# Optimization experiments

Hardware: AMD Instinct MI355X
Metric: run time of the kernel (lower is better)

The kernel has to match this reference:

```python
import math
import jax, jax.numpy as jnp
import numpy as np

B, S, D, H, DH, R, V = 8, 1024, 1024, 8, 512, 36, 32002  # DH = d_model//2, HD = h*DH = 4096
HD = H * DH
LN_EPS = 1e-5


def setup_inputs() -> dict:
    key = jax.random.key(0)
    ks = jax.random.split(key, 16)

    def n(k, shp, std=0.02):
        return jax.random.normal(k, shp, jnp.float32) * std

    pre_words = jax.random.randint(ks[0], (B, S), 0, V)
    img_features = jax.random.normal(ks[1], (B, R, D), jnp.float32)
    exp_embed = n(ks[2], (V, D)).at[0].set(0.0)  # padding_idx=0
    # id2visual table: sparse nonneg rows over 36 regions; zero rows -> textual tokens
    id2vis = (jax.random.uniform(ks[3], (V, R)) < 0.05).astype(jnp.float32)
    # stacked params for 2 transformer layers; weights stored (in, out) so y = x @ W + b
    wq = n(ks[4], (2, D, HD)); bq = jnp.zeros((2, HD), jnp.float32)
    wk = n(ks[5], (2, D, HD)); bk = jnp.zeros((2, HD), jnp.float32)
    wv = n(ks[6], (2, D, HD)); bv = jnp.zeros((2, HD), jnp.float32)
    wo = n(ks[7], (2, HD, D)); bo = jnp.zeros((2, D), jnp.float32)
    w1 = n(ks[8], (2, D, D)); b1 = jnp.zeros((2, D), jnp.float32)
    w2 = n(ks[9], (2, D, D)); b2 = jnp.zeros((2, D), jnp.float32)
    ln1_g = jnp.ones((2, D), jnp.float32); ln1_b = jnp.zeros((2, D), jnp.float32)
    ln2_g = jnp.ones((2, D), jnp.float32); ln2_b = jnp.zeros((2, D), jnp.float32)
    return dict(pre_words=pre_words, img_features=img_features, exp_embed=exp_embed,
                id2vis=id2vis, wq=wq, bq=bq, wk=wk, bk=bk, wv=wv, bv=bv, wo=wo, bo=bo,
                w1=w1, b1=b1, w2=w2, b2=b2, ln1_g=ln1_g, ln1_b=ln1_b, ln2_g=ln2_g, ln2_b=ln2_b)


def _layer_norm(x, g, b):
    m = x.mean(-1, keepdims=True)
    v = ((x - m) ** 2).mean(-1, keepdims=True)
    return (x - m) / jnp.sqrt(v + LN_EPS) * g + b


def _softmax_one(x):
    # shifted-denominator softmax: exp(x - max) / (1 + sum exp(x - max))
    x = x - x.max(-1, keepdims=True)
    e = jnp.exp(x)
    return e / (1.0 + e.sum(-1, keepdims=True))


def reference(pre_words, img_features, exp_embed, id2vis, wq, bq, wk, bk, wv, bv,
              wo, bo, w1, b1, w2, b2, ln1_g, ln1_b, ln2_g, ln2_b):
    # token embedding: textual (masked to 0 where a visual row exists) + visual bmm
    te = exp_embed[pre_words]                       # (B,S,D)
    vids = id2vis[pre_words]                        # (B,S,R)
    word_mask = vids.sum(-1, keepdims=True) != 0    # (B,S,1)
    ve = jnp.einsum('bsr,brd->bsd', vids, img_features)
    x = jnp.where(word_mask, 0.0, te) + ve          # (B,S,D)

    scale = 1.0 / math.sqrt(DH)
    for i in range(2):  # two structurally identical transformer layers
        h = _layer_norm(x, ln1_g[i], ln1_b[i])
        q = (h @ wq[i] + bq[i]).reshape(B, S, H, DH).transpose(0, 2, 1, 3)
        k = (h @ wk[i] + bk[i]).reshape(B, S, H, DH).transpose(0, 2, 1, 3)
        v = (h @ wv[i] + bv[i]).reshape(B, S, H, DH).transpose(0, 2, 1, 3)
        attn = _softmax_one(jnp.einsum('bhqd,bhkd->bhqk', q, k) * scale)  # (B,H,S,S)
        o = jnp.einsum('bhqk,bhkd->bhqd', attn, v)
        o = o.transpose(0, 2, 1, 3).reshape(B, S, HD)
        x = x + (o @ wo[i] + bo[i])
        f = _layer_norm(x, ln2_g[i], ln2_b[i])
        f = jax.nn.gelu(f @ w1[i] + b1[i], approximate=False) @ w2[i] + b2[i]
        x = x + f
    return x
```

## Files before the change

kernel.cpp:

```cpp
#include <hip/hip_runtime.h>


using u16 = unsigned short;
typedef __attribute__((ext_vector_type(8))) short bf16x8;
typedef __attribute__((ext_vector_type(4))) float f32x4;

__device__ __forceinline__ float b2f(u16 u) {
  union { unsigned int i; float f; } v; v.i = ((unsigned int)u) << 16; return v.f;
}
__device__ __forceinline__ u16 f2b(float f) {
  union { float f; unsigned int i; } v; v.f = f;
  unsigned int i = v.i;
  return (u16)((i + 0x7FFFu + ((i >> 16) & 1u)) >> 16);
}
__device__ __forceinline__ float gelu_f(float x) {
  return 0.5f * x * (1.f + erff(x * 0.70710678118654752f));
}
__device__ __forceinline__ void async16(void* lds, const void* g) {
  __builtin_amdgcn_global_load_lds((const __attribute__((address_space(1))) void*)g,
                                   (__attribute__((address_space(3))) void*)lds, 16, 0, 0);
}
__device__ __forceinline__ void storeC(float* p, float v) { *p = v; }
__device__ __forceinline__ void storeC(u16* p, float v) { *p = f2b(v); }

__global__ __launch_bounds__(256) void embed_k(
    const int* __restrict__ words, const float* __restrict__ img,
    const float* __restrict__ emb, const float* __restrict__ id2v,
    float* __restrict__ x)
{
  __shared__ float vs[36];
  int tok = blockIdx.x, b = tok >> 10, t = threadIdx.x;
  int wd = words[tok];
  if (t < 36) vs[t] = id2v[(size_t)wd * 36 + t];
  __syncthreads();
  bool any = false;
#pragma unroll
  for (int r = 0; r < 36; ++r) any = any || (vs[r] != 0.f);
#pragma unroll
  for (int i = 0; i < 4; ++i) {
    int d = t + (i << 8);
    float acc = 0.f;
    for (int r = 0; r < 36; ++r) {
      float vv = vs[r];
      if (vv != 0.f) acc += vv * img[((size_t)(b * 36 + r) << 10) + d];
    }
    float te = any ? 0.f : emb[((size_t)wd << 10) + d];
    x[((size_t)tok << 10) + d] = te + acc;
  }
}

__global__ __launch_bounds__(256) void ln_k(
    const float* __restrict__ x, u16* __restrict__ out,
    const float* __restrict__ g, const float* __restrict__ bb)
{
  __shared__ float red[4];
  int row = blockIdx.x, t = threadIdx.x;
  const float* xr = x + ((size_t)row << 10);
  float v[4], s = 0.f;
#pragma unroll
  for (int i = 0; i < 4; ++i) { v[i] = xr[t + (i << 8)]; s += v[i]; }
#pragma unroll
  for (int o = 32; o; o >>= 1) s += __shfl_xor(s, o, 64);
  if ((t & 63) == 0) red[t >> 6] = s;
  __syncthreads();
  s = red[0] + red[1] + red[2] + red[3];
  float mean = s * 0.0009765625f;
  float q = 0.f;
#pragma unroll
  for (int i = 0; i < 4; ++i) { float d = v[i] - mean; q += d * d; }
  __syncthreads();
#pragma unroll
  for (int o = 32; o; o >>= 1) q += __shfl_xor(q, o, 64);
  if ((t & 63) == 0) red[t >> 6] = q;
  __syncthreads();
  q = red[0] + red[1] + red[2] + red[3];
  float rstd = rsqrtf(q * 0.0009765625f + 1e-5f);
  u16* orow = out + ((size_t)row << 10);
#pragma unroll
  for (int i = 0; i < 4; ++i) {
    int d = t + (i << 8);
    orow[d] = f2b((v[i] - mean) * rstd * g[d] + bb[d]);
  }
}

__global__ __launch_bounds__(256) void sm_k(const float* __restrict__ S, u16* __restrict__ P)
{
  __shared__ float red[4];
  size_t row = blockIdx.x;
  int t = threadIdx.x;
  const float* sr = S + (row << 10);
  float v[4], m = -3.0e38f;
#pragma unroll
  for (int i = 0; i < 4; ++i) { v[i] = sr[t + (i << 8)]; m = fmaxf(m, v[i]); }
#pragma unroll
  for (int o = 32; o; o >>= 1) m = fmaxf(m, __shfl_xor(m, o, 64));
  if ((t & 63) == 0) red[t >> 6] = m;
  __syncthreads();
  m = fmaxf(fmaxf(red[0], red[1]), fmaxf(red[2], red[3]));
  float e[4], s = 0.f;
#pragma unroll
  for (int i = 0; i < 4; ++i) { e[i] = __expf(v[i] - m); s += e[i]; }
  __syncthreads();
#pragma unroll
  for (int o = 32; o; o >>= 1) s += __shfl_xor(s, o, 64);
  if ((t & 63) == 0) red[t >> 6] = s;
  __syncthreads();
  s = red[0] + red[1] + red[2] + red[3];
  float inv = 1.f / (1.f + s);
  u16* pr = P + (row << 10);
#pragma unroll
  for (int i = 0; i < 4; ++i) pr[t + (i << 8)] = f2b(e[i] * inv);
}

__global__ __launch_bounds__(256) void tr_k(
    const float* __restrict__ src, u16* __restrict__ dst, int ls, int ld)
{
  __shared__ u16 tile[64][65];
  int c0 = blockIdx.x << 6, r0 = blockIdx.y << 6;
  int tx = threadIdx.x & 63, ty0 = threadIdx.x >> 6;
#pragma unroll
  for (int i = 0; i < 16; ++i) {
    int ty = (ty0 << 4) + i;
    tile[ty][tx] = f2b(src[(size_t)(r0 + ty) * ls + (c0 + tx)]);
  }
  __syncthreads();
#pragma unroll
  for (int i = 0; i < 16; ++i) {
    int ty = (ty0 << 4) + i;
    dst[(size_t)(c0 + ty) * ld + (r0 + tx)] = tile[tx][ty];
  }
}

template <typename CT, int ACT, int BIAS, int RESID>
__global__ __launch_bounds__(256, 4) void gemm128(
    const u16* __restrict__ A, const u16* __restrict__ Bt,
    CT* __restrict__ C, const float* __restrict__ bias,
    const float* __restrict__ resid,
    int M, int N, int K, int lda, int ldb, int ldc, float scale,
    int zbase, int zdiv, int ga, int gb, int gc,
    long long aS1, long long aS2, long long bS1, long long bS2,
    long long cS1, long long cS2)
{
  __shared__ u16 lA[128 * 64];
  __shared__ u16 lB[128 * 64];
  const int nwg = gridDim.x * gridDim.y;
  const int id = blockIdx.y * gridDim.x + blockIdx.x;
  const int qq = nwg >> 3, rr8 = nwg & 7;
  const int xcd = id & 7, off = id >> 3;
  const int swz = (xcd < rr8 ? xcd * (qq + 1) : rr8 * (qq + 1) + (xcd - rr8) * qq) + off;
  const int bx = swz % gridDim.x, by = swz / gridDim.x;

  long long lz = blockIdx.z;
  long long gz = zbase + lz;
  long long zA = ga ? gz : lz, zB = gb ? gz : lz, zC = gc ? gz : lz;
  size_t aOff = (size_t)((zA / zdiv) * aS1 + (zA % zdiv) * aS2);
  size_t bOff = (size_t)((zB / zdiv) * bS1 + (zB % zdiv) * bS2);
  size_t cOff = (size_t)((zC / zdiv) * cS1 + (zC % zdiv) * cS2);
  const int m0 = by << 7, n0 = bx << 7;
  const int tid = threadIdx.x, lane = tid & 63, w = tid >> 6;
  const int wm = w >> 1, wn = w & 1;
  const int srow8 = lane >> 3;
  const int schunk = (lane & 7) ^ srow8;
  const int fr = lane & 15, hi = lane >> 4;

  f32x4 acc[4][4];
#pragma unroll
  for (int mi = 0; mi < 4; ++mi)
#pragma unroll
    for (int ni = 0; ni < 4; ++ni) acc[mi][ni] = 0.f;

  const u16* Ab = A + aOff;
  const u16* Bb = Bt + bOff;

  for (int k0 = 0; k0 < K; k0 += 64) {
#pragma unroll
    for (int s = 0; s < 4; ++s) {
      const int rb = (s << 5) + (w << 3);
      async16(&lA[rb << 6], Ab + (size_t)(m0 + rb + srow8) * lda + (k0 + (schunk << 3)));
      async16(&lB[rb << 6], Bb + (size_t)(n0 + rb + srow8) * ldb + (k0 + (schunk << 3)));
    }
    __syncthreads();
#pragma unroll
    for (int ks = 0; ks < 2; ++ks) {
      const int q = (ks << 2) + hi;
      bf16x8 a8[4], b8[4];
#pragma unroll
      for (int mi = 0; mi < 4; ++mi) {
        const int R = (wm << 6) + (mi << 4) + fr;
        a8[mi] = *(const bf16x8*)&lA[(R << 6) + ((q ^ (R & 7)) << 3)];
      }
#pragma unroll
      for (int ni = 0; ni < 4; ++ni) {
        const int R = (wn << 6) + (ni << 4) + fr;
        b8[ni] = *(const bf16x8*)&lB[(R << 6) + ((q ^ (R & 7)) << 3)];
      }
#pragma unroll
      for (int mi = 0; mi < 4; ++mi)
#pragma unroll
        for (int ni = 0; ni < 4; ++ni)
          acc[mi][ni] = __builtin_amdgcn_mfma_f32_16x16x32_bf16(a8[mi], b8[ni], acc[mi][ni], 0, 0, 0);
    }
    __syncthreads();
  }

  const int r4 = hi << 2, cc = fr;
#pragma unroll
  for (int mi = 0; mi < 4; ++mi) {
#pragma unroll
    for (int ni = 0; ni < 4; ++ni) {
      const int col = n0 + (wn << 6) + (ni << 4) + cc;
      float bcol = 0.f;
      if (BIAS == 1) bcol = bias[col];
#pragma unroll
      for (int j = 0; j < 4; ++j) {
        const int row = m0 + (wm << 6) + (mi << 4) + r4 + j;
        float v = acc[mi][ni][j] * scale + bcol;
        if (BIAS == 2) v += bias[row];
        if (ACT == 1) v = gelu_f(v);
        const size_t idx = cOff + (size_t)row * ldc + col;
        if (RESID) v += resid[idx];
        storeC(&C[idx], v);
      }
    }
  }
}

extern "C" void kernel_launch(void* const* d_in, const int* in_sizes, int n_in,
                              void* d_out, int out_size, void* d_ws, size_t ws_size,
                              hipStream_t stream)
{
  (void)in_sizes; (void)n_in; (void)out_size;
  const int*   pre_words = (const int*)d_in[0];
  const float* img  = (const float*)d_in[1];
  const float* emb  = (const float*)d_in[2];
  const float* id2v = (const float*)d_in[3];
  const float* wq = (const float*)d_in[4];  const float* bq = (const float*)d_in[5];
  const float* wk = (const float*)d_in[6];  const float* bk = (const float*)d_in[7];
  const float* wv = (const float*)d_in[8];  const float* bv = (const float*)d_in[9];
  const float* wo = (const float*)d_in[10]; const float* bo = (const float*)d_in[11];
  const float* w1 = (const float*)d_in[12]; const float* b1 = (const float*)d_in[13];
  const float* w2 = (const float*)d_in[14]; const float* b2 = (const float*)d_in[15];
  const float* ln1g = (const float*)d_in[16]; const float* ln1b = (const float*)d_in[17];
  const float* ln2g = (const float*)d_in[18]; const float* ln2b = (const float*)d_in[19];

  const size_t FIXED = 88080384 + (size_t)(1 << 16);
  int g = 1;
  for (int c = 8; c >= 1; c >>= 1)
    if (FIXED + (size_t)c * 33554432 + 6291456 <= ws_size) { g = c; break; }
  int nc = 1;
  int ncmax = 8 * g > 32 ? 32 : 8 * g;
  for (int c = ncmax; c >= 1; c >>= 1)
    if (FIXED + (size_t)g * 33554432 + (size_t)c * 6291456 <= ws_size) { nc = c; break; }

  char* p = (char*)d_ws;
  auto alloc = [&](size_t bytes) -> void* {
    void* r = (void*)p; p += (bytes + 255) & ~(size_t)255; return r;
  };
  float* x  = (float*)alloc((size_t)8192 * 1024 * 4);
  u16* h    = (u16*)alloc((size_t)8192 * 1024 * 2);
  u16* Qg   = (u16*)alloc((size_t)g * 1024 * 4096 * 2);
  u16* Og   = (u16*)alloc((size_t)g * 1024 * 4096 * 2);
  u16* ff   = Qg;
  u16* Kg   = (u16*)alloc((size_t)g * 1024 * 4096 * 2);
  u16* Vtg  = (u16*)alloc((size_t)g * 4096 * 1024 * 2);
  u16* wqt  = (u16*)alloc((size_t)4096 * 1024 * 2);
  u16* wkt  = (u16*)alloc((size_t)4096 * 1024 * 2);
  u16* wvt  = (u16*)alloc((size_t)4096 * 1024 * 2);
  u16* wot  = (u16*)alloc((size_t)1024 * 4096 * 2);
  u16* w1t  = (u16*)alloc((size_t)1024 * 1024 * 2);
  u16* w2t  = (u16*)alloc((size_t)1024 * 1024 * 2);
  float* Sc = (float*)alloc((size_t)nc << 22);
  u16*  Pp  = (u16*)alloc((size_t)nc << 21);

  embed_k<<<8192, 256, 0, stream>>>(pre_words, img, emb, id2v, x);

  const float qk_scale = 0.044194173824159216f;
  for (int L = 0; L < 2; ++L) {
    const float* WQ = wq + (size_t)L * 1024 * 4096;
    const float* WK = wk + (size_t)L * 1024 * 4096;
    const float* WV = wv + (size_t)L * 1024 * 4096;
    const float* WO = wo + (size_t)L * 4096 * 1024;
    const float* W1 = w1 + (size_t)L * 1024 * 1024;
    const float* W2 = w2 + (size_t)L * 1024 * 1024;

    tr_k<<<dim3(64, 16), 256, 0, stream>>>(WQ, wqt, 4096, 1024);
    tr_k<<<dim3(64, 16), 256, 0, stream>>>(WK, wkt, 4096, 1024);
    tr_k<<<dim3(64, 16), 256, 0, stream>>>(WV, wvt, 4096, 1024);
    tr_k<<<dim3(16, 64), 256, 0, stream>>>(WO, wot, 1024, 4096);
    tr_k<<<dim3(16, 16), 256, 0, stream>>>(W1, w1t, 1024, 1024);
    tr_k<<<dim3(16, 16), 256, 0, stream>>>(W2, w2t, 1024, 1024);

    ln_k<<<8192, 256, 0, stream>>>(x, h, ln1g + L * 1024, ln1b + L * 1024);

    for (int g0 = 0; g0 < 8; g0 += g) {
      const u16* hg = h + (size_t)g0 * 1048576;
      const int Mg = 1024 * g;
      gemm128<u16, 0, 1, 0><<<dim3(32, Mg >> 7), 256, 0, stream>>>(
          hg, wqt, Qg, bq + (size_t)L * 4096, nullptr,
          Mg, 4096, 1024, 1024, 1024, 4096, 1.f,
          0, 1, 0, 0, 0, 0, 0, 0, 0, 0, 0);
      gemm128<u16, 0, 1, 0><<<dim3(32, Mg >> 7), 256, 0, stream>>>(
          hg, wkt, Kg, bk + (size_t)L * 4096, nullptr,
          Mg, 4096, 1024, 1024, 1024, 4096, 1.f,
          0, 1, 0, 0, 0, 0, 0, 0, 0, 0, 0);
      gemm128<u16, 0, 2, 0><<<dim3(8, 32, g), 256, 0, stream>>>(
          wvt, h, Vtg, bv + (size_t)L * 4096, nullptr,
          4096, 1024, 1024, 1024, 1024, 1024, 1.f,
          g0, 1, 0, 1, 0, 0, 0, 1048576LL, 0, 4194304LL, 0);
      for (int c0 = 0; c0 < 8 * g; c0 += nc) {
        gemm128<float, 0, 0, 0><<<dim3(8, 8, nc), 256, 0, stream>>>(
            Qg, Kg, Sc, nullptr, nullptr,
            1024, 1024, 512, 4096, 4096, 1024, qk_scale,
            c0, 8, 1, 1, 0,
            4194304LL, 512LL, 4194304LL, 512LL, 8388608LL, 1048576LL);
        sm_k<<<nc << 10, 256, 0, stream>>>(Sc, Pp);
        gemm128<u16, 0, 0, 0><<<dim3(4, 8, nc), 256, 0, stream>>>(
            Pp, Vtg, Og, nullptr, nullptr,
            1024, 512, 1024, 1024, 1024, 4096, 1.f,
            c0, 8, 0, 1, 1,
            8388608LL, 1048576LL, 4194304LL, 524288LL, 4194304LL, 512LL);
      }
      gemm128<float, 0, 1, 1><<<dim3(8, Mg >> 7), 256, 0, stream>>>(
          Og, wot, x + (size_t)g0 * 1048576, bo + (size_t)L * 1024,
          x + (size_t)g0 * 1048576,
          Mg, 1024, 4096, 4096, 4096, 1024, 1.f,
          0, 1, 0, 0, 0, 0, 0, 0, 0, 0, 0);
    }

    ln_k<<<8192, 256, 0, stream>>>(x, h, ln2g + L * 1024, ln2b + L * 1024);

    gemm128<u16, 1, 1, 0><<<dim3(8, 64), 256, 0, stream>>>(
        h, w1t, ff, b1 + (size_t)L * 1024, nullptr,
        8192, 1024, 1024, 1024, 1024, 1024, 1.f,
        0, 1, 0, 0, 0, 0, 0, 0, 0, 0, 0);
    float* cdst = (L == 1) ? (float*)d_out : x;
    gemm128<float, 0, 1, 1><<<dim3(8, 64), 256, 0, stream>>>(
        ff, w2t, cdst, b2 + (size_t)L * 1024, x,
        8192, 1024, 1024, 1024, 1024, 1024, 1.f,
        0, 1, 0, 0, 0, 0, 0, 0, 0, 0, 0);
  }
}
```

Before: 1.655 ms.

## Store attention scores in bf16, vectorize softmax, add 128x64 GEMM tiles

The QK^T score buffer is now written as bf16 instead of fp32, which halves score write and softmax read traffic and frees workspace for larger chunk counts. The softmax kernel now loads and stores four contiguous elements per thread with ushort4. The GEMM is templated on N-tile width: N=1024 projections (Wo, FFN) use 128x64 tiles for more workgroups, and launch-bound occupancy hints are raised. Rounding scores to bf16 before softmax adds some precision loss.

```diff
diff --git a/kernel.cpp b/kernel.cpp
--- a/kernel.cpp
+++ b/kernel.cpp
@@ -83,15 +83,15 @@
   }
 }
 
-__global__ __launch_bounds__(256) void sm_k(const float* __restrict__ S, u16* __restrict__ P)
+__global__ __launch_bounds__(256) void sm_k(const u16* __restrict__ S, u16* __restrict__ P)
 {
   __shared__ float red[4];
   size_t row = blockIdx.x;
   int t = threadIdx.x;
-  const float* sr = S + (row << 10);
-  float v[4], m = -3.0e38f;
-#pragma unroll
-  for (int i = 0; i < 4; ++i) { v[i] = sr[t + (i << 8)]; m = fmaxf(m, v[i]); }
+  const u16* sr = S + (row << 10);
+  ushort4 sv = *(const ushort4*)(sr + (t << 2));
+  float v[4] = { b2f(sv.x), b2f(sv.y), b2f(sv.z), b2f(sv.w) };
+  float m = fmaxf(fmaxf(v[0], v[1]), fmaxf(v[2], v[3]));
 #pragma unroll
   for (int o = 32; o; o >>= 1) m = fmaxf(m, __shfl_xor(m, o, 64));
   if ((t & 63) == 0) red[t >> 6] = m;
@@ -107,9 +107,10 @@
   __syncthreads();
   s = red[0] + red[1] + red[2] + red[3];
   float inv = 1.f / (1.f + s);
-  u16* pr = P + (row << 10);
-#pragma unroll
-  for (int i = 0; i < 4; ++i) pr[t + (i << 8)] = f2b(e[i] * inv);
+  ushort4 pv;
+  pv.x = f2b(e[0] * inv); pv.y = f2b(e[1] * inv);
+  pv.z = f2b(e[2] * inv); pv.w = f2b(e[3] * inv);
+  *(ushort4*)(P + (row << 10) + (t << 2)) = pv;
 }
 
 __global__ __launch_bounds__(256) void tr_k(
@@ -131,8 +132,8 @@
   }
 }
 
-template <typename CT, int ACT, int BIAS, int RESID>
-__global__ __launch_bounds__(256, 4) void gemm128(
+template <typename CT, int ACT, int BIAS, int RESID, int BN>
+__global__ __launch_bounds__(256, (BN == 128) ? 5 : 6) void gemm_t(
     const u16* __restrict__ A, const u16* __restrict__ Bt,
     CT* __restrict__ C, const float* __restrict__ bias,
     const float* __restrict__ resid,
@@ -141,8 +142,9 @@
     long long aS1, long long aS2, long long bS1, long long bS2,
     long long cS1, long long cS2)
 {
+  constexpr int NACC = BN / 32;
   __shared__ u16 lA[128 * 64];
-  __shared__ u16 lB[128 * 64];
+  __shared__ u16 lB[BN * 64];
   const int nwg = gridDim.x * gridDim.y;
   const int id = blockIdx.y * gridDim.x + blockIdx.x;
   const int qq = nwg >> 3, rr8 = nwg & 7;
@@ -156,18 +158,18 @@
   size_t aOff = (size_t)((zA / zdiv) * aS1 + (zA % zdiv) * aS2);
   size_t bOff = (size_t)((zB / zdiv) * bS1 + (zB % zdiv) * bS2);
   size_t cOff = (size_t)((zC / zdiv) * cS1 + (zC % zdiv) * cS2);
-  const int m0 = by << 7, n0 = bx << 7;
+  const int m0 = by << 7, n0 = bx * BN;
   const int tid = threadIdx.x, lane = tid & 63, w = tid >> 6;
   const int wm = w >> 1, wn = w & 1;
   const int srow8 = lane >> 3;
   const int schunk = (lane & 7) ^ srow8;
   const int fr = lane & 15, hi = lane >> 4;
 
-  f32x4 acc[4][4];
+  f32x4 acc[4][NACC];
 #pragma unroll
   for (int mi = 0; mi < 4; ++mi)
 #pragma unroll
-    for (int ni = 0; ni < 4; ++ni) acc[mi][ni] = 0.f;
+    for (int ni = 0; ni < NACC; ++ni) acc[mi][ni] = 0.f;
 
   const u16* Ab = A + aOff;
   const u16* Bb = Bt + bOff;
@@ -177,27 +179,31 @@
     for (int s = 0; s < 4; ++s) {
       const int rb = (s << 5) + (w << 3);
       async16(&lA[rb << 6], Ab + (size_t)(m0 + rb + srow8) * lda + (k0 + (schunk << 3)));
+    }
+#pragma unroll
+    for (int s = 0; s < BN / 32; ++s) {
+      const int rb = (s << 5) + (w << 3);
       async16(&lB[rb << 6], Bb + (size_t)(n0 + rb + srow8) * ldb + (k0 + (schunk << 3)));
     }
     __syncthreads();
 #pragma unroll
     for (int ks = 0; ks < 2; ++ks) {
       const int q = (ks << 2) + hi;
-      bf16x8 a8[4], b8[4];
+      bf16x8 a8[4], b8[NACC];
 #pragma unroll
       for (int mi = 0; mi < 4; ++mi) {
         const int R = (wm << 6) + (mi << 4) + fr;
         a8[mi] = *(const bf16x8*)&lA[(R << 6) + ((q ^ (R & 7)) << 3)];
       }
 #pragma unroll
-      for (int ni = 0; ni < 4; ++ni) {
-        const int R = (wn << 6) + (ni << 4) + fr;
+      for (int ni = 0; ni < NACC; ++ni) {
+        const int R = wn * (BN / 2) + (ni << 4) + fr;
         b8[ni] = *(const bf16x8*)&lB[(R << 6) + ((q ^ (R & 7)) << 3)];
       }
 #pragma unroll
       for (int mi = 0; mi < 4; ++mi)
 #pragma unroll
-        for (int ni = 0; ni < 4; ++ni)
+        for (int ni = 0; ni < NACC; ++ni)
           acc[mi][ni] = __builtin_amdgcn_mfma_f32_16x16x32_bf16(a8[mi], b8[ni], acc[mi][ni], 0, 0, 0);
     }
     __syncthreads();
@@ -207,8 +213,8 @@
 #pragma unroll
   for (int mi = 0; mi < 4; ++mi) {
 #pragma unroll
-    for (int ni = 0; ni < 4; ++ni) {
-      const int col = n0 + (wn << 6) + (ni << 4) + cc;
+    for (int ni = 0; ni < NACC; ++ni) {
+      const int col = n0 + wn * (BN / 2) + (ni << 4) + cc;
       float bcol = 0.f;
       if (BIAS == 1) bcol = bias[col];
 #pragma unroll
@@ -246,11 +252,11 @@
   const size_t FIXED = 88080384 + (size_t)(1 << 16);
   int g = 1;
   for (int c = 8; c >= 1; c >>= 1)
-    if (FIXED + (size_t)c * 33554432 + 6291456 <= ws_size) { g = c; break; }
+    if (FIXED + (size_t)c * 33554432 + 4194304 <= ws_size) { g = c; break; }
   int nc = 1;
   int ncmax = 8 * g > 32 ? 32 : 8 * g;
   for (int c = ncmax; c >= 1; c >>= 1)
-    if (FIXED + (size_t)g * 33554432 + (size_t)c * 6291456 <= ws_size) { nc = c; break; }
+    if (FIXED + (size_t)g * 33554432 + (size_t)c * 4194304 <= ws_size) { nc = c; break; }
 
   char* p = (char*)d_ws;
   auto alloc = [&](size_t bytes) -> void* {
@@ -269,8 +275,8 @@
   u16* wot  = (u16*)alloc((size_t)1024 * 4096 * 2);
   u16* w1t  = (u16*)alloc((size_t)1024 * 1024 * 2);
   u16* w2t  = (u16*)alloc((size_t)1024 * 1024 * 2);
-  float* Sc = (float*)alloc((size_t)nc << 22);
-  u16*  Pp  = (u16*)alloc((size_t)nc << 21);
+  u16* Sc   = (u16*)alloc((size_t)nc << 21);
+  u16* Pp   = (u16*)alloc((size_t)nc << 21);
 
   embed_k<<<8192, 256, 0, stream>>>(pre_words, img, emb, id2v, x);
 
@@ -295,32 +301,32 @@
     for (int g0 = 0; g0 < 8; g0 += g) {
       const u16* hg = h + (size_t)g0 * 1048576;
       const int Mg = 1024 * g;
-      gemm128<u16, 0, 1, 0><<<dim3(32, Mg >> 7), 256, 0, stream>>>(
+      gemm_t<u16, 0, 1, 0, 128><<<dim3(32, Mg >> 7), 256, 0, stream>>>(
           hg, wqt, Qg, bq + (size_t)L * 4096, nullptr,
           Mg, 4096, 1024, 1024, 1024, 4096, 1.f,
           0, 1, 0, 0, 0, 0, 0, 0, 0, 0, 0);
-      gemm128<u16, 0, 1, 0><<<dim3(32, Mg >> 7), 256, 0, stream>>>(
+      gemm_t<u16, 0, 1, 0, 128><<<dim3(32, Mg >> 7), 256, 0, stream>>>(
           hg, wkt, Kg, bk + (size_t)L * 4096, nullptr,
           Mg, 4096, 1024, 1024, 1024, 4096, 1.f,
           0, 1, 0, 0, 0, 0, 0, 0, 0, 0, 0);
-      gemm128<u16, 0, 2, 0><<<dim3(8, 32, g), 256, 0, stream>>>(
+      gemm_t<u16, 0, 2, 0, 128><<<dim3(8, 32, g), 256, 0, stream>>>(
           wvt, h, Vtg, bv + (size_t)L * 4096, nullptr,
           4096, 1024, 1024, 1024, 1024, 1024, 1.f,
           g0, 1, 0, 1, 0, 0, 0, 1048576LL, 0, 4194304LL, 0);
       for (int c0 = 0; c0 < 8 * g; c0 += nc) {
-        gemm128<float, 0, 0, 0><<<dim3(8, 8, nc), 256, 0, stream>>>(
+        gemm_t<u16, 0, 0, 0, 128><<<dim3(8, 8, nc), 256, 0, stream>>>(
             Qg, Kg, Sc, nullptr, nullptr,
             1024, 1024, 512, 4096, 4096, 1024, qk_scale,
             c0, 8, 1, 1, 0,
             4194304LL, 512LL, 4194304LL, 512LL, 8388608LL, 1048576LL);
         sm_k<<<nc << 10, 256, 0, stream>>>(Sc, Pp);
-        gemm128<u16, 0, 0, 0><<<dim3(4, 8, nc), 256, 0, stream>>>(
+        gemm_t<u16, 0, 0, 0, 128><<<dim3(4, 8, nc), 256, 0, stream>>>(
             Pp, Vtg, Og, nullptr, nullptr,
             1024, 512, 1024, 1024, 1024, 4096, 1.f,
             c0, 8, 0, 1, 1,
             8388608LL, 1048576LL, 4194304LL, 524288LL, 4194304LL, 512LL);
       }
-      gemm128<float, 0, 1, 1><<<dim3(8, Mg >> 7), 256, 0, stream>>>(
+      gemm_t<float, 0, 1, 1, 64><<<dim3(16, Mg >> 7), 256, 0, stream>>>(
           Og, wot, x + (size_t)g0 * 1048576, bo + (size_t)L * 1024,
           x + (size_t)g0 * 1048576,
           Mg, 1024, 4096, 4096, 4096, 1024, 1.f,
@@ -329,12 +335,12 @@
 
     ln_k<<<8192, 256, 0, stream>>>(x, h, ln2g + L * 1024, ln2b + L * 1024);
 
-    gemm128<u16, 1, 1, 0><<<dim3(8, 64), 256, 0, stream>>>(
+    gemm_t<u16, 1, 1, 0, 64><<<dim3(16, 64), 256, 0, stream>>>(
         h, w1t, ff, b1 + (size_t)L * 1024, nullptr,
         8192, 1024, 1024, 1024, 1024, 1024, 1.f,
         0, 1, 0, 0, 0, 0, 0, 0, 0, 0, 0);
     float* cdst = (L == 1) ? (float*)d_out : x;
-    gemm128<float, 0, 1, 1><<<dim3(8, 64), 256, 0, stream>>>(
+    gemm_t<float, 0, 1, 1, 64><<<dim3(16, 64), 256, 0, stream>>>(
         ff, w2t, cdst, b2 + (size_t)L * 1024, x,
         8192, 1024, 1024, 1024, 1024, 1024, 1.f,
         0, 1, 0, 0, 0, 0, 0, 0, 0, 0, 0);
```

After: 2.734 ms. +65.2%, slower.
